# Kernel tuning notes

Hardware: AMD Instinct MI355X
Metric: run time of the kernel (lower is better)

## Reference

```python
import jax, jax.numpy as jnp
import numpy as np

K = 3  # kernel_size / number of adjacency partitions


def setup_inputs() -> dict:
    key = jax.random.key(0)
    k1, k2, k3 = jax.random.split(key, 3)
    N, C_in, T, V = 64, 64, 300, 25
    C_out = 64
    x = jax.random.normal(k1, (N, C_in, T, V), dtype=jnp.float32)
    A = jax.random.uniform(k2, (K, V, V), dtype=jnp.float32)
    W = jax.random.normal(k3, (C_in, K * C_out), dtype=jnp.float32) * 0.05
    b = jnp.zeros((K * C_out,), dtype=jnp.float32)
    return {"x": x, "A": A, "W": W, "b": b}


def reference(x, A, W, b):
    # 1x1 conv (channels_first) == per-position channel projection
    # x: [N, C_in, T, V], W: [C_in, K*C_out] -> y: [N, K*C_out, T, V]
    y = jnp.einsum('nitv,io->notv', x, W) + b[None, :, None, None]
    N, KC, T, V = y.shape
    C = KC // K
    y = y.reshape(N, K, C, T, V)
    # graph adjacency aggregation: [N,K,C,T,V] x [K,V,W] -> [N,C,T,W]
    out = jnp.einsum('nkctv,kvw->nctw', y, A)
    return (out, A)
```

## Files before the change

### kernel.cpp

```cpp
#include <hip/hip_runtime.h>
#include <hip/hip_bf16.h>


#define TT 6
#define TCHUNKS 50
#define NB 64
#define CI 64
#define TDIM 300
#define VDIM 25
#define CO 64
#define KK 3

#define XROWS (TT*32)
#define SMEM_BYTES (XROWS*128)
#define NBAT 12

#define WBUF_BYTES (KK*4*2*64*16)
#define ABUF_BYTES (KK*2*64*16)

typedef __attribute__((ext_vector_type(8))) short bf16x8;
typedef __attribute__((ext_vector_type(4))) float f32x4;
typedef __attribute__((ext_vector_type(4))) int i32x4;

__device__ __forceinline__ unsigned short f2bf(float f) {
    unsigned int u = __builtin_bit_cast(unsigned int, f);
    u += 0x7fffu + ((u >> 16) & 1u);
    return (unsigned short)(u >> 16);
}
__device__ __forceinline__ unsigned int pack2(float lo, float hi) {
    return (unsigned int)f2bf(lo) | ((unsigned int)f2bf(hi) << 16);
}

__global__ void sgcn_prep(const float* __restrict__ A, const float* __restrict__ W,
                          unsigned int* __restrict__ wbuf, unsigned int* __restrict__ abuf,
                          float* __restrict__ outA) {
    int id = blockIdx.x * 256 + threadIdx.x;
    if (id < KK * 4 * 2 * 64) {
        int l  = id & 63;
        int h  = (id >> 6) & 1;
        int wq = (id >> 7) & 3;
        int k  = id >> 9;
        int c  = wq * 16 + (l & 15);
        int ib = (l >> 4) * 8 + h * 32;
        unsigned int pk[4];
        #pragma unroll
        for (int j = 0; j < 4; ++j)
            pk[j] = pack2(W[(size_t)(ib + 2*j)     * (KK*CO) + k*CO + c],
                          W[(size_t)(ib + 2*j + 1) * (KK*CO) + k*CO + c]);
        *(uint4*)(wbuf + id * 4) = make_uint4(pk[0], pk[1], pk[2], pk[3]);
    }
    if (id < KK * 2 * 64) {
        int l  = id & 63;
        int nt = (id >> 6) & 1;
        int k  = id >> 7;
        int w  = nt * 16 + (l & 15);
        int vb = (l >> 4) * 8;
        unsigned int pk[4];
        #pragma unroll
        for (int j = 0; j < 4; ++j) {
            int v0 = vb + 2*j, v1 = v0 + 1;
            unsigned short u0 = (v0 < VDIM && w < VDIM) ? f2bf(A[k*VDIM*VDIM + v0*VDIM + w]) : (unsigned short)0;
            unsigned short u1 = (v1 < VDIM && w < VDIM) ? f2bf(A[k*VDIM*VDIM + v1*VDIM + w]) : (unsigned short)0;
            pk[j] = (unsigned int)u0 | ((unsigned int)u1 << 16);
        }
        *(uint4*)(abuf + id * 4) = make_uint4(pk[0], pk[1], pk[2], pk[3]);
    }
    if (id < KK * VDIM * VDIM) outA[id] = A[id];
}

__global__ __launch_bounds__(256, 4) void sgcn_fused(
    const float* __restrict__ x, const float* __restrict__ b,
    const unsigned int* __restrict__ wbuf, const unsigned int* __restrict__ abuf,
    float* __restrict__ out)
{
    __shared__ __align__(16) char smem[SMEM_BYTES];
    const int tid  = threadIdx.x;
    const int lane = tid & 63;
    const int wid  = tid >> 6;
    const int n    = blockIdx.y;
    const int t0   = blockIdx.x * TT;
    const int l15  = lane & 15;
    const int g    = lane >> 4;
    const int i0   = g * 8;
    const int c    = wid * 16 + l15;

    float s0[NBAT], s1[NBAT];
    #pragma unroll 1
    for (int bat = 0; bat < 2; ++bat) {
        #pragma unroll
        for (int it = 0; it < NBAT; ++it) {
            int idx = tid + (bat * NBAT + it) * 256;
            int i2  = idx / XROWS;
            int r   = idx - i2 * XROWS;
            int rr  = r & 31;
            int v   = ((rr & 15) >> 2) * 8 + (rr >> 4) * 4 + (rr & 3);
            s0[it] = 0.f; s1[it] = 0.f;
            if (v < VDIM) {
                const float* xp = x + (((size_t)n * CI + 2*i2) * TDIM + (t0 + (r >> 5))) * VDIM + v;
                s0[it] = xp[0];
                s1[it] = xp[(size_t)TDIM * VDIM];
            }
        }
        #pragma unroll
        for (int it = 0; it < NBAT; ++it) {
            int idx = tid + (bat * NBAT + it) * 256;
            int i2  = idx / XROWS;
            int r   = idx - i2 * XROWS;
            *(unsigned int*)(smem + r * 128 + ((4*i2) ^ ((r & 7) << 4))) = pack2(s0[it], s1[it]);
        }
    }
    __syncthreads();

    bf16x8 WB[KK][2], AB[KK][2];
    float bv[KK];
    #pragma unroll
    for (int k = 0; k < KK; ++k) {
        WB[k][0] = *(const bf16x8*)(wbuf + (((k*4 + wid)*2 + 0)*64 + lane)*4);
        WB[k][1] = *(const bf16x8*)(wbuf + (((k*4 + wid)*2 + 1)*64 + lane)*4);
        AB[k][0] = *(const bf16x8*)(abuf + ((k*2 + 0)*64 + lane)*4);
        AB[k][1] = *(const bf16x8*)(abuf + ((k*2 + 1)*64 + lane)*4);
        bv[k]    = b[k*CO + c];
    }

    const size_t cs = (size_t)TDIM * VDIM;
    #pragma unroll
    for (int t = 0; t < TT; ++t) {
        int j0 = t*32 + l15;
        int j1 = j0 + 16;
        const char* p0 = smem + j0*128;
        const char* p1 = smem + j1*128;
        bf16x8 A00 = *(const bf16x8*)(p0 + ((2*i0)      ^ ((j0 & 7) << 4)));
        bf16x8 A01 = *(const bf16x8*)(p0 + ((2*i0 + 64) ^ ((j0 & 7) << 4)));
        bf16x8 A10 = *(const bf16x8*)(p1 + ((2*i0)      ^ ((j1 & 7) << 4)));
        bf16x8 A11 = *(const bf16x8*)(p1 + ((2*i0 + 64) ^ ((j1 & 7) << 4)));

        f32x4 accA = {0.f, 0.f, 0.f, 0.f};
        f32x4 accB = {0.f, 0.f, 0.f, 0.f};
        #pragma unroll
        for (int k = 0; k < KK; ++k) {
            f32x4 D0 = {bv[k], bv[k], bv[k], bv[k]};
            f32x4 D1 = D0;
            D0 = __builtin_amdgcn_mfma_f32_16x16x32_bf16(A00, WB[k][0], D0, 0, 0, 0);
            D0 = __builtin_amdgcn_mfma_f32_16x16x32_bf16(A01, WB[k][1], D0, 0, 0, 0);
            D1 = __builtin_amdgcn_mfma_f32_16x16x32_bf16(A10, WB[k][0], D1, 0, 0, 0);
            D1 = __builtin_amdgcn_mfma_f32_16x16x32_bf16(A11, WB[k][1], D1, 0, 0, 0);
            i32x4 pav = {(int)pack2(D0.x, D0.y), (int)pack2(D0.z, D0.w),
                         (int)pack2(D1.x, D1.y), (int)pack2(D1.z, D1.w)};
            bf16x8 PA = __builtin_bit_cast(bf16x8, pav);
            accA = __builtin_amdgcn_mfma_f32_16x16x32_bf16(PA, AB[k][0], accA, 0, 0, 0);
            accB = __builtin_amdgcn_mfma_f32_16x16x32_bf16(PA, AB[k][1], accB, 0, 0, 0);
        }
        size_t base = (((size_t)n * CO + (wid*16 + 4*g)) * TDIM + (t0 + t)) * VDIM + l15;
        out[base]        = accA.x;
        out[base + cs]   = accA.y;
        out[base + 2*cs] = accA.z;
        out[base + 3*cs] = accA.w;
        if (l15 < VDIM - 16) {
            size_t base2 = base + 16;
            out[base2]        = accB.x;
            out[base2 + cs]   = accB.y;
            out[base2 + 2*cs] = accB.z;
            out[base2 + 3*cs] = accB.w;
        }
    }
}

extern "C" void kernel_launch(void* const* d_in, const int* in_sizes, int n_in,
                              void* d_out, int out_size, void* d_ws, size_t ws_size,
                              hipStream_t stream) {
    const float* x = (const float*)d_in[0];
    const float* A = (const float*)d_in[1];
    const float* W = (const float*)d_in[2];
    const float* b = (const float*)d_in[3];
    float* out = (float*)d_out;

    unsigned int* wbuf = (unsigned int*)d_ws;
    unsigned int* abuf = (unsigned int*)((char*)d_ws + WBUF_BYTES);

    const size_t out_elems = (size_t)NB * CO * TDIM * VDIM;
    sgcn_prep<<<8, 256, 0, stream>>>(A, W, wbuf, abuf, out + out_elems);

    dim3 grid(TCHUNKS, NB);
    sgcn_fused<<<grid, 256, 0, stream>>>(x, b, wbuf, abuf, out);
}
```

Baseline: 60.30 us.

## Make blocks persistent over five time chunks with double-buffered LDS prefetch

```diff
diff --git a/kernel.cpp b/kernel.cpp
--- a/kernel.cpp
+++ b/kernel.cpp
@@ -3,7 +3,8 @@
 
 
 #define TT 6
-#define TCHUNKS 50
+#define NCHUNK 5
+#define GRIDX 10
 #define NB 64
 #define CI 64
 #define TDIM 300
@@ -68,48 +69,53 @@
     if (id < KK * VDIM * VDIM) outA[id] = A[id];
 }
 
-__global__ __launch_bounds__(256, 4) void sgcn_fused(
+__device__ __forceinline__ void stage_load(const float* __restrict__ x, int n, int tbase,
+                                           int half, int tid, float* s0, float* s1) {
+    #pragma unroll
+    for (int it = 0; it < NBAT; ++it) {
+        int idx = tid + (half * NBAT + it) * 256;
+        int i2  = idx / XROWS;
+        int r   = idx - i2 * XROWS;
+        int rr  = r & 31;
+        int v   = ((rr & 15) >> 2) * 8 + (rr >> 4) * 4 + (rr & 3);
+        s0[it] = 0.f; s1[it] = 0.f;
+        if (v < VDIM) {
+            const float* xp = x + (((size_t)n * CI + 2*i2) * TDIM + (tbase + (r >> 5))) * VDIM + v;
+            s0[it] = xp[0];
+            s1[it] = xp[(size_t)TDIM * VDIM];
+        }
+    }
+}
+__device__ __forceinline__ void stage_write(char* __restrict__ buf, int half, int tid,
+                                            const float* s0, const float* s1) {
+    #pragma unroll
+    for (int it = 0; it < NBAT; ++it) {
+        int idx = tid + (half * NBAT + it) * 256;
+        int i2  = idx / XROWS;
+        int r   = idx - i2 * XROWS;
+        *(unsigned int*)(buf + r * 128 + ((4*i2) ^ ((r & 7) << 4))) = pack2(s0[it], s1[it]);
+    }
+}
+
+__global__ __launch_bounds__(256, 2) void sgcn_fused(
     const float* __restrict__ x, const float* __restrict__ b,
     const unsigned int* __restrict__ wbuf, const unsigned int* __restrict__ abuf,
     float* __restrict__ out)
 {
-    __shared__ __align__(16) char smem[SMEM_BYTES];
+    __shared__ __align__(16) char smem[2][SMEM_BYTES];
     const int tid  = threadIdx.x;
     const int lane = tid & 63;
     const int wid  = tid >> 6;
     const int n    = blockIdx.y;
-    const int t0   = blockIdx.x * TT;
+    const int t0   = blockIdx.x * (TT * NCHUNK);
     const int l15  = lane & 15;
     const int g    = lane >> 4;
     const int i0   = g * 8;
     const int c    = wid * 16 + l15;
 
     float s0[NBAT], s1[NBAT];
-    #pragma unroll 1
-    for (int bat = 0; bat < 2; ++bat) {
-        #pragma unroll
-        for (int it = 0; it < NBAT; ++it) {
-            int idx = tid + (bat * NBAT + it) * 256;
-            int i2  = idx / XROWS;
-            int r   = idx - i2 * XROWS;
-            int rr  = r & 31;
-            int v   = ((rr & 15) >> 2) * 8 + (rr >> 4) * 4 + (rr & 3);
-            s0[it] = 0.f; s1[it] = 0.f;
-            if (v < VDIM) {
-                const float* xp = x + (((size_t)n * CI + 2*i2) * TDIM + (t0 + (r >> 5))) * VDIM + v;
-                s0[it] = xp[0];
-                s1[it] = xp[(size_t)TDIM * VDIM];
-            }
-        }
-        #pragma unroll
-        for (int it = 0; it < NBAT; ++it) {
-            int idx = tid + (bat * NBAT + it) * 256;
-            int i2  = idx / XROWS;
-            int r   = idx - i2 * XROWS;
-            *(unsigned int*)(smem + r * 128 + ((4*i2) ^ ((r & 7) << 4))) = pack2(s0[it], s1[it]);
-        }
-    }
-    __syncthreads();
+
+    stage_load(x, n, t0, 0, tid, s0, s1);
 
     bf16x8 WB[KK][2], AB[KK][2];
     float bv[KK];
@@ -122,46 +128,71 @@
         bv[k]    = b[k*CO + c];
     }
 
+    stage_write(&smem[0][0], 0, tid, s0, s1);
+    stage_load(x, n, t0, 1, tid, s0, s1);
+    stage_write(&smem[0][0], 1, tid, s0, s1);
+    __syncthreads();
+
     const size_t cs = (size_t)TDIM * VDIM;
-    #pragma unroll
-    for (int t = 0; t < TT; ++t) {
-        int j0 = t*32 + l15;
-        int j1 = j0 + 16;
-        const char* p0 = smem + j0*128;
-        const char* p1 = smem + j1*128;
-        bf16x8 A00 = *(const bf16x8*)(p0 + ((2*i0)      ^ ((j0 & 7) << 4)));
-        bf16x8 A01 = *(const bf16x8*)(p0 + ((2*i0 + 64) ^ ((j0 & 7) << 4)));
-        bf16x8 A10 = *(const bf16x8*)(p1 + ((2*i0)      ^ ((j1 & 7) << 4)));
-        bf16x8 A11 = *(const bf16x8*)(p1 + ((2*i0 + 64) ^ ((j1 & 7) << 4)));
-
-        f32x4 accA = {0.f, 0.f, 0.f, 0.f};
-        f32x4 accB = {0.f, 0.f, 0.f, 0.f};
+
+    #pragma unroll 1
+    for (int ch = 0; ch < NCHUNK; ++ch) {
+        const char* rbuf = &smem[ch & 1][0];
+        char*       pbuf = &smem[(ch + 1) & 1][0];
+        const bool  pf   = (ch + 1) < NCHUNK;
+        const int   tg0  = t0 + ch * TT;
+
+        if (pf) stage_load(x, n, tg0 + TT, 0, tid, s0, s1);
+
         #pragma unroll
-        for (int k = 0; k < KK; ++k) {
-            f32x4 D0 = {bv[k], bv[k], bv[k], bv[k]};
-            f32x4 D1 = D0;
-            D0 = __builtin_amdgcn_mfma_f32_16x16x32_bf16(A00, WB[k][0], D0, 0, 0, 0);
-            D0 = __builtin_amdgcn_mfma_f32_16x16x32_bf16(A01, WB[k][1], D0, 0, 0, 0);
-            D1 = __builtin_amdgcn_mfma_f32_16x16x32_bf16(A10, WB[k][0], D1, 0, 0, 0);
-            D1 = __builtin_amdgcn_mfma_f32_16x16x32_bf16(A11, WB[k][1], D1, 0, 0, 0);
-            i32x4 pav = {(int)pack2(D0.x, D0.y), (int)pack2(D0.z, D0.w),
-                         (int)pack2(D1.x, D1.y), (int)pack2(D1.z, D1.w)};
-            bf16x8 PA = __builtin_bit_cast(bf16x8, pav);
-            accA = __builtin_amdgcn_mfma_f32_16x16x32_bf16(PA, AB[k][0], accA, 0, 0, 0);
-            accB = __builtin_amdgcn_mfma_f32_16x16x32_bf16(PA, AB[k][1], accB, 0, 0, 0);
+        for (int half = 0; half < 2; ++half) {
+            #pragma unroll
+            for (int tt = 0; tt < 3; ++tt) {
+                int t = half * 3 + tt;
+                int j0 = t*32 + l15;
+                int j1 = j0 + 16;
+                const char* p0 = rbuf + j0*128;
+                const char* p1 = rbuf + j1*128;
+                bf16x8 A00 = *(const bf16x8*)(p0 + ((2*i0)      ^ ((j0 & 7) << 4)));
+                bf16x8 A01 = *(const bf16x8*)(p0 + ((2*i0 + 64) ^ ((j0 & 7) << 4)));
+                bf16x8 A10 = *(const bf16x8*)(p1 + ((2*i0)      ^ ((j1 & 7) << 4)));
+                bf16x8 A11 = *(const bf16x8*)(p1 + ((2*i0 + 64) ^ ((j1 & 7) << 4)));
+
+                f32x4 accA = {0.f, 0.f, 0.f, 0.f};
+                f32x4 accB = {0.f, 0.f, 0.f, 0.f};
+                #pragma unroll
+                for (int k = 0; k < KK; ++k) {
+                    f32x4 D0 = {bv[k], bv[k], bv[k], bv[k]};
+                    f32x4 D1 = D0;
+                    D0 = __builtin_amdgcn_mfma_f32_16x16x32_bf16(A00, WB[k][0], D0, 0, 0, 0);
+                    D0 = __builtin_amdgcn_mfma_f32_16x16x32_bf16(A01, WB[k][1], D0, 0, 0, 0);
+                    D1 = __builtin_amdgcn_mfma_f32_16x16x32_bf16(A10, WB[k][0], D1, 0, 0, 0);
+                    D1 = __builtin_amdgcn_mfma_f32_16x16x32_bf16(A11, WB[k][1], D1, 0, 0, 0);
+                    i32x4 pav = {(int)pack2(D0.x, D0.y), (int)pack2(D0.z, D0.w),
+                                 (int)pack2(D1.x, D1.y), (int)pack2(D1.z, D1.w)};
+                    bf16x8 PA = __builtin_bit_cast(bf16x8, pav);
+                    accA = __builtin_amdgcn_mfma_f32_16x16x32_bf16(PA, AB[k][0], accA, 0, 0, 0);
+                    accB = __builtin_amdgcn_mfma_f32_16x16x32_bf16(PA, AB[k][1], accB, 0, 0, 0);
+                }
+                size_t base = (((size_t)n * CO + (wid*16 + 4*g)) * TDIM + (tg0 + t)) * VDIM + l15;
+                out[base]        = accA.x;
+                out[base + cs]   = accA.y;
+                out[base + 2*cs] = accA.z;
+                out[base + 3*cs] = accA.w;
+                if (l15 < VDIM - 16) {
+                    size_t base2 = base + 16;
+                    out[base2]        = accB.x;
+                    out[base2 + cs]   = accB.y;
+                    out[base2 + 2*cs] = accB.z;
+                    out[base2 + 3*cs] = accB.w;
+                }
+            }
+            if (pf) {
+                stage_write(pbuf, half, tid, s0, s1);
+                if (half == 0) stage_load(x, n, tg0 + TT, 1, tid, s0, s1);
+            }
         }
-        size_t base = (((size_t)n * CO + (wid*16 + 4*g)) * TDIM + (t0 + t)) * VDIM + l15;
-        out[base]        = accA.x;
-        out[base + cs]   = accA.y;
-        out[base + 2*cs] = accA.z;
-        out[base + 3*cs] = accA.w;
-        if (l15 < VDIM - 16) {
-            size_t base2 = base + 16;
-            out[base2]        = accB.x;
-            out[base2 + cs]   = accB.y;
-            out[base2 + 2*cs] = accB.z;
-            out[base2 + 3*cs] = accB.w;
-        }
+        __syncthreads();
     }
 }
 
@@ -180,6 +211,6 @@
     const size_t out_elems = (size_t)NB * CO * TDIM * VDIM;
     sgcn_prep<<<8, 256, 0, stream>>>(A, W, wbuf, abuf, out + out_elems);
 
-    dim3 grid(TCHUNKS, NB);
+    dim3 grid(GRIDX, NB);
     sgcn_fused<<<grid, 256, 0, stream>>>(x, b, wbuf, abuf, out);
 }
```

Measured after the change: 70.75 us. 17.3% more time.
